# Kernel tuning notes

Hardware: AMD Instinct MI355X
Metric: run time of the kernel (lower is better)

The kernel has to match this reference:

```python
import jax, jax.numpy as jnp
import numpy as np

K = 3        # kernel_size
DIL = 1      # dilation
PAD = 1      # padding (replicate)
RANKS = 3
STAGES = 9
C_OUT = 32


def setup_inputs() -> dict:
    key = jax.random.key(0)
    k1, k2, k3 = jax.random.split(key, 3)
    b, cin, H, W = 2, 3, 160, 160
    x = jax.random.normal(k1, (b, cin, H, W), dtype=jnp.float32)
    head_w = jax.random.normal(k2, (C_OUT, cin), dtype=jnp.float32) * (1.0 / np.sqrt(cin))
    tail_w = jax.random.normal(k3, (cin, C_OUT), dtype=jnp.float32) * (1.0 / np.sqrt(C_OUT))
    alphas = jnp.full((STAGES,), 0.01, dtype=jnp.float32)
    betas = jnp.full((STAGES,), 0.01, dtype=jnp.float32)
    return {"x": x, "head_w": head_w, "tail_w": tail_w, "alphas": alphas, "betas": betas}


def _unfold_like_torch(xp, H, W):
    # xp: [b, C, H+2p, W+2p] replicate-padded. Reproduce torch nn.Unfold output
    # layout [b, C*k*k, H*W] (channel-major, then ki, kj; L row-major over h,w).
    b, C = xp.shape[0], xp.shape[1]
    cols = [xp[:, :, i * DIL:i * DIL + H, j * DIL:j * DIL + W]
            for i in range(K) for j in range(K)]
    patches = jnp.stack(cols, axis=2)            # [b, C, k*k, H, W]
    return patches.reshape(b, C * K * K, H * W)  # torch unfold layout


def reference(x, head_w, tail_w, alphas, betas):
    b, cin, H, W = x.shape
    # head 1x1 conv (no bias) + relu
    xh = jax.nn.relu(jnp.einsum('bchw,oc->bohw', x, head_w))
    xp = jnp.pad(xh, ((0, 0), (0, 0), (PAD, PAD), (PAD, PAD)), mode='edge')
    Xu = _unfold_like_torch(xp, H, W)                 # [b, C*kk, H*W]
    # Faithful to torch: X = unfold.view(b, C, H, W, -1) (row-major reinterpret)
    X = Xu.reshape(b, C_OUT, H, W, K * K)
    U = jnp.repeat(X.mean(axis=-1, keepdims=True), RANKS, axis=-1)  # [b,C,H,W,r]
    V = jnp.repeat(X.mean(axis=1, keepdims=True), RANKS, axis=1)    # [b,r,H,W,kk]
    for i in range(STAGES):
        num_V = jnp.einsum('bchwr,bchwk->brhwk', U, X)
        UV = jnp.einsum('bchwr,brhwk->bchwk', U, V)
        den_V = jnp.einsum('bchwr,bchwk->brhwk', U, UV)
        V = V - betas[i] * (den_V - num_V)
        num_U = jnp.einsum('bchwk,brhwk->bchwr', X, V)
        UV = jnp.einsum('bchwr,brhwk->bchwk', U, V)
        den_U = jnp.einsum('bchwk,brhwk->bchwr', UV, V)
        U = U - alphas[i] * (den_U - num_U)
    center = (K // 2) * K + K // 2
    UVc = jnp.einsum('bchwr,brhwk->bchwk', U, V)[..., center]  # [b,C,H,W]
    out = jax.nn.relu(jnp.einsum('bchw,oc->bohw', UVc, tail_w))
    return out
```

## Files before the change

### kernel.cpp

```cpp
#include <hip/hip_runtime.h>
#include <hip/hip_bf16.h>

#define NB    2
#define HW    25600
#define WDIM  160
#define NSTG  9

template <int CTRL>
__device__ __forceinline__ float dpp_add(float v) {
    int moved = __builtin_amdgcn_update_dpp(0, __float_as_int(v), CTRL, 0xf, 0xf, true);
    return v + __int_as_float(moved);
}

__device__ __forceinline__ float reduce4(float v) {
    v = dpp_add<0xB1>(v);
    v = dpp_add<0x4E>(v);
    return v;
}

__device__ __forceinline__ constexpr int hidx(int i, int j) {
    return (i <= j) ? (9 * i - (i * (i - 1)) / 2 + (j - i))
                    : (9 * j - (j * (j - 1)) / 2 + (i - j));
}

__global__ __launch_bounds__(256, 3) void fused_kernel(const float* __restrict__ x,
                                                       const float* __restrict__ head_w,
                                                       const float* __restrict__ tail_w,
                                                       const float* __restrict__ alphas,
                                                       const float* __restrict__ betas,
                                                       float* __restrict__ out) {
    int sub = threadIdx.x & 3;
    int pid = blockIdx.x * 64 + (threadIdx.x >> 2);
    int b   = blockIdx.x / 400;
    int s2  = pid - b * HW;
    int c0  = sub * 8;

    float al[NSTG], be[NSTG];
#pragma unroll
    for (int i = 0; i < NSTG; ++i) { al[i] = alphas[i]; be[i] = betas[i]; }

    const float* xb0 = x + b * 3 * HW;

    int g9  = s2 * 9;
    int kk0 = g9 / HW;
    int r0  = g9 - kk0 * HW;
    int h0  = r0 / WDIM;
    int w0  = r0 - h0 * WDIM;
    int ki0 = kk0 / 3;
    int dh0 = ki0 - 1,            dw0 = kk0 - ki0 * 3 - 1;
    int kk1 = kk0 + 1;
    int ki1 = kk1 / 3;
    int dh1 = ki1 - 1,            dw1 = kk1 - ki1 * 3 - 1;

    int p[9];
#pragma unroll
    for (int k2 = 0; k2 < 9; ++k2) {
        int r  = r0 + k2;
        int wn = w0 + k2;
        int cw = (wn >= WDIM);
        int w1 = cw ? wn - WDIM : wn;
        int h1 = h0 + cw;
        bool wr = (r >= HW);
        int h  = wr ? 0 : h1;
        int w  = wr ? r - HW : w1;
        int dh = wr ? dh1 : dh0;
        int dw = wr ? dw1 : dw0;
        int hh = min(max(h + dh, 0), 159);
        int ww = min(max(w + dw, 0), 159);
        p[k2]  = hh * WDIM + ww;
    }

    float xv0[9], xv1[9], xv2[9];
#pragma unroll
    for (int k2 = 0; k2 < 9; ++k2) xv0[k2] = xb0[p[k2]];
#pragma unroll
    for (int k2 = 0; k2 < 9; ++k2) xv1[k2] = xb0[HW + p[k2]];
#pragma unroll
    for (int k2 = 0; k2 < 9; ++k2) xv2[k2] = xb0[2 * HW + p[k2]];

    float X[9][8];
#pragma unroll
    for (int j = 0; j < 8; ++j) {
        float hwj0 = head_w[(c0 + j) * 3 + 0];
        float hwj1 = head_w[(c0 + j) * 3 + 1];
        float hwj2 = head_w[(c0 + j) * 3 + 2];
#pragma unroll
        for (int k2 = 0; k2 < 9; ++k2)
            X[k2][j] = fmaxf(hwj0 * xv0[k2] + hwj1 * xv1[k2] + hwj2 * xv2[k2], 0.f);
    }

    float Hm[45];
#pragma unroll
    for (int i = 0; i < 9; ++i) {
#pragma unroll
        for (int j = i; j < 9; ++j) {
            float hp = ((X[i][0] * X[j][0] + X[i][1] * X[j][1])
                      + (X[i][2] * X[j][2] + X[i][3] * X[j][3]))
                     + ((X[i][4] * X[j][4] + X[i][5] * X[j][5])
                      + (X[i][6] * X[j][6] + X[i][7] * X[j][7]));
            Hm[hidx(i, j)] = reduce4(hp);
        }
    }

    float v[9];
#pragma unroll
    for (int k = 0; k < 9; ++k) {
        float pr = ((X[k][0] + X[k][1]) + (X[k][2] + X[k][3]))
                 + ((X[k][4] + X[k][5]) + (X[k][6] + X[k][7]));
        v[k] = reduce4(pr) * (1.f / 32.f);
    }
    float a[9];
#pragma unroll
    for (int k = 0; k < 9; ++k) a[k] = (1.f / 9.f);

#pragma unroll
    for (int i = 0; i < NSTG; ++i) {
        float beta  = be[i];
        float alpha = al[i];
        float b3 = 3.f * beta;
        float a3 = 3.f * alpha;
        float c[9];
#pragma unroll
        for (int r = 0; r < 9; ++r) {
            float t0 = Hm[hidx(r, 0)] * a[0] + Hm[hidx(r, 1)] * a[1];
            float t1 = Hm[hidx(r, 2)] * a[2] + Hm[hidx(r, 3)] * a[3];
            float t2 = Hm[hidx(r, 4)] * a[4] + Hm[hidx(r, 5)] * a[5];
            float t3 = Hm[hidx(r, 6)] * a[6] + Hm[hidx(r, 7)] * a[7];
            c[r] = ((t0 + t1) + (t2 + t3)) + Hm[hidx(r, 8)] * a[8];
        }
        float S = (((a[0] * c[0] + a[1] * c[1]) + (a[2] * c[2] + a[3] * c[3]))
                +  ((a[4] * c[4] + a[5] * c[5]) + (a[6] * c[6] + a[7] * c[7])))
                +  a[8] * c[8];
        float vs = 1.f - b3 * S;
#pragma unroll
        for (int k = 0; k < 9; ++k)
            v[k] = v[k] * vs + beta * c[k];
        float T = (((v[0] * v[0] + v[1] * v[1]) + (v[2] * v[2] + v[3] * v[3]))
                +  ((v[4] * v[4] + v[5] * v[5]) + (v[6] * v[6] + v[7] * v[7])))
                +  v[8] * v[8];
        float us = 1.f - a3 * T;
#pragma unroll
        for (int k = 0; k < 9; ++k)
            a[k] = a[k] * us + alpha * v[k];
    }

    float v4 = v[4];
    float uvc[8];
#pragma unroll
    for (int j = 0; j < 8; ++j) {
        float t0 = X[0][j] * a[0] + X[1][j] * a[1];
        float t1 = X[2][j] * a[2] + X[3][j] * a[3];
        float t2 = X[4][j] * a[4] + X[5][j] * a[5];
        float t3 = X[6][j] * a[6] + X[7][j] * a[7];
        float u  = ((t0 + t1) + (t2 + t3)) + X[8][j] * a[8];
        uvc[j] = 3.f * u * v4;
    }
    float o[3];
#pragma unroll
    for (int oo = 0; oo < 3; ++oo) {
        const float* tw = tail_w + oo * 32 + c0;
        float pr = ((uvc[0] * tw[0] + uvc[1] * tw[1]) + (uvc[2] * tw[2] + uvc[3] * tw[3]))
                 + ((uvc[4] * tw[4] + uvc[5] * tw[5]) + (uvc[6] * tw[6] + uvc[7] * tw[7]));
        o[oo] = fmaxf(reduce4(pr), 0.f);
    }
    if (sub == 0) {
        float* op = out + b * 3 * HW + s2;
        op[0]      = o[0];
        op[HW]     = o[1];
        op[2 * HW] = o[2];
    }
}

extern "C" void kernel_launch(void* const* d_in, const int* in_sizes, int n_in,
                              void* d_out, int out_size, void* d_ws, size_t ws_size,
                              hipStream_t stream) {
    const float* x      = (const float*)d_in[0];
    const float* head_w = (const float*)d_in[1];
    const float* tail_w = (const float*)d_in[2];
    const float* alphas = (const float*)d_in[3];
    const float* betas  = (const float*)d_in[4];
    float*       out    = (float*)d_out;

    fused_kernel<<<dim3(NB * HW * 4 / 256), dim3(256), 0, stream>>>(
        x, head_w, tail_w, alphas, betas, out);
}
```

Measured before the change: 81.33 us.

## Stream channels into Gram accumulators and precompute tail projection to drop X array

The 9x8 X activation array is no longer kept live. Each channel's 9 values are computed on the fly and accumulated into the Gram matrix, the channel-sum vector, and a 3x9 tail-weighted projection Gp. The final output then contracts Gp with a instead of rebuilding per-channel uvc. This reorders the algebra, (tail·X)·a instead of tail·(X·a), and aims to cut register pressure (72 live X values replaced by 27 Gp values) and final-stage work. The cost is 27 extra accumulators carried through the channel loop and some change in floating-point summation order.

New measurement: 80.52 us. Within noise of the previous version (-1.0%).

```diff
diff --git a/kernel.cpp b/kernel.cpp
--- a/kernel.cpp
+++ b/kernel.cpp
@@ -78,37 +78,58 @@
 #pragma unroll
     for (int k2 = 0; k2 < 9; ++k2) xv2[k2] = xb0[2 * HW + p[k2]];
 
-    float X[9][8];
-#pragma unroll
-    for (int j = 0; j < 8; ++j) {
-        float hwj0 = head_w[(c0 + j) * 3 + 0];
-        float hwj1 = head_w[(c0 + j) * 3 + 1];
-        float hwj2 = head_w[(c0 + j) * 3 + 2];
-#pragma unroll
-        for (int k2 = 0; k2 < 9; ++k2)
-            X[k2][j] = fmaxf(hwj0 * xv0[k2] + hwj1 * xv1[k2] + hwj2 * xv2[k2], 0.f);
-    }
-
-    float Hm[45];
-#pragma unroll
-    for (int i = 0; i < 9; ++i) {
-#pragma unroll
-        for (int j = i; j < 9; ++j) {
-            float hp = ((X[i][0] * X[j][0] + X[i][1] * X[j][1])
-                      + (X[i][2] * X[j][2] + X[i][3] * X[j][3]))
-                     + ((X[i][4] * X[j][4] + X[i][5] * X[j][5])
-                      + (X[i][6] * X[j][6] + X[i][7] * X[j][7]));
-            Hm[hidx(i, j)] = reduce4(hp);
+    float Hm[45], v0p[9], Gp[3][9];
+    {
+        float w0h = head_w[c0 * 3 + 0];
+        float w1h = head_w[c0 * 3 + 1];
+        float w2h = head_w[c0 * 3 + 2];
+        float Xc[9];
+#pragma unroll
+        for (int k = 0; k < 9; ++k)
+            Xc[k] = fmaxf(w0h * xv0[k] + w1h * xv1[k] + w2h * xv2[k], 0.f);
+#pragma unroll
+        for (int i = 0; i < 9; ++i)
+#pragma unroll
+            for (int jj = i; jj < 9; ++jj)
+                Hm[hidx(i, jj)] = Xc[i] * Xc[jj];
+#pragma unroll
+        for (int k = 0; k < 9; ++k) v0p[k] = Xc[k];
+#pragma unroll
+        for (int oo = 0; oo < 3; ++oo) {
+            float tw = tail_w[oo * 32 + c0];
+#pragma unroll
+            for (int k = 0; k < 9; ++k) Gp[oo][k] = tw * Xc[k];
         }
     }
-
+#pragma unroll
+    for (int j = 1; j < 8; ++j) {
+        float w0h = head_w[(c0 + j) * 3 + 0];
+        float w1h = head_w[(c0 + j) * 3 + 1];
+        float w2h = head_w[(c0 + j) * 3 + 2];
+        float Xc[9];
+#pragma unroll
+        for (int k = 0; k < 9; ++k)
+            Xc[k] = fmaxf(w0h * xv0[k] + w1h * xv1[k] + w2h * xv2[k], 0.f);
+#pragma unroll
+        for (int i = 0; i < 9; ++i)
+#pragma unroll
+            for (int jj = i; jj < 9; ++jj)
+                Hm[hidx(i, jj)] += Xc[i] * Xc[jj];
+#pragma unroll
+        for (int k = 0; k < 9; ++k) v0p[k] += Xc[k];
+#pragma unroll
+        for (int oo = 0; oo < 3; ++oo) {
+            float tw = tail_w[oo * 32 + c0 + j];
+#pragma unroll
+            for (int k = 0; k < 9; ++k) Gp[oo][k] += tw * Xc[k];
+        }
+    }
+
+#pragma unroll
+    for (int t = 0; t < 45; ++t) Hm[t] = reduce4(Hm[t]);
     float v[9];
 #pragma unroll
-    for (int k = 0; k < 9; ++k) {
-        float pr = ((X[k][0] + X[k][1]) + (X[k][2] + X[k][3]))
-                 + ((X[k][4] + X[k][5]) + (X[k][6] + X[k][7]));
-        v[k] = reduce4(pr) * (1.f / 32.f);
-    }
+    for (int k = 0; k < 9; ++k) v[k] = reduce4(v0p[k]) * (1.f / 32.f);
     float a[9];
 #pragma unroll
     for (int k = 0; k < 9; ++k) a[k] = (1.f / 9.f);
@@ -145,23 +166,16 @@
     }
 
     float v4 = v[4];
-    float uvc[8];
-#pragma unroll
-    for (int j = 0; j < 8; ++j) {
-        float t0 = X[0][j] * a[0] + X[1][j] * a[1];
-        float t1 = X[2][j] * a[2] + X[3][j] * a[3];
-        float t2 = X[4][j] * a[4] + X[5][j] * a[5];
-        float t3 = X[6][j] * a[6] + X[7][j] * a[7];
-        float u  = ((t0 + t1) + (t2 + t3)) + X[8][j] * a[8];
-        uvc[j] = 3.f * u * v4;
-    }
     float o[3];
 #pragma unroll
     for (int oo = 0; oo < 3; ++oo) {
-        const float* tw = tail_w + oo * 32 + c0;
-        float pr = ((uvc[0] * tw[0] + uvc[1] * tw[1]) + (uvc[2] * tw[2] + uvc[3] * tw[3]))
-                 + ((uvc[4] * tw[4] + uvc[5] * tw[5]) + (uvc[6] * tw[6] + uvc[7] * tw[7]));
-        o[oo] = fmaxf(reduce4(pr), 0.f);
+        float t0 = Gp[oo][0] * a[0] + Gp[oo][1] * a[1];
+        float t1 = Gp[oo][2] * a[2] + Gp[oo][3] * a[3];
+        float t2 = Gp[oo][4] * a[4] + Gp[oo][5] * a[5];
+        float t3 = Gp[oo][6] * a[6] + Gp[oo][7] * a[7];
+        float d  = ((t0 + t1) + (t2 + t3)) + Gp[oo][8] * a[8];
+        float r  = reduce4(d);
+        o[oo] = fmaxf(3.f * v4 * r, 0.f);
     }
     if (sub == 0) {
         float* op = out + b * 3 * HW + s2;
```
